# Kernel tuning notes

Hardware: AMD Instinct MI355X
Metric: run time of the kernel (lower is better)

## Reference

```python
import jax, jax.numpy as jnp
import numpy as np

W_ENTROPY, W_MI, W_COV, W_ORTHO, W_L1, W_L2 = 1.0, 0.2, 0.2, 0.1, 0.1, 0.1


def setup_inputs() -> dict:
    key = jax.random.key(0)
    k1, k2, k3, k4 = jax.random.split(key, 4)
    B, NCLS, C = 16384, 1000, 1280
    logits = jax.random.normal(k1, (B, NCLS), dtype=jnp.float32)
    output = jax.nn.log_softmax(logits, axis=1)  # nll_loss expects log-probs
    target = jax.random.randint(k2, (B,), 0, NCLS, dtype=jnp.int64)
    weights = jax.random.normal(k3, (NCLS, C), dtype=jnp.float32) * 0.02
    features = jax.random.normal(k4, (B, C), dtype=jnp.float32)
    return {"output": output, "target": target, "weights": weights, "features": features}


def _kl_loss(features):
    # torch: sum_{i,j} F.kl_div(L[:, i], L[:, j], log_target=True, reduction='mean')
    # kl_div(input, tgt, log_target=True) = mean_b exp(tgt)*(tgt - input)
    # => sum_{i,j,b} P[b,j]*(L[b,j]-L[b,i]) / B
    #  = (C * sum(P*L) - sum(L)) / B   (since sum_j P[b,j] == 1)
    B, C = features.shape
    L = jax.nn.log_softmax(features, axis=1)
    P = jnp.exp(L)
    return (C * jnp.sum(P * L) - jnp.sum(L)) / B


def _cov_loss(features):
    B = features.shape[0]
    cf = features - jnp.mean(features, axis=0, keepdims=True)
    cov = (cf.T @ cf) / B  # [C, C]
    eye = jnp.eye(cov.shape[0], dtype=cov.dtype)
    return jnp.sum((cov - eye) ** 2)  # ||.||_F^2


def _ortho_loss(weights):
    w = weights.reshape(weights.shape[0], -1)
    cov = w @ w.T  # row type
    eye = jnp.eye(cov.shape[0], dtype=cov.dtype)
    return jnp.sum((cov - eye) ** 2)


def reference(output, target, weights, features):
    loss_nll = -jnp.mean(jnp.take_along_axis(output, target[:, None], axis=1))
    loss_kl = _kl_loss(features)
    loss_cov = _cov_loss(features)
    loss_ortho = _ortho_loss(weights)
    loss_l1 = jnp.sum(jnp.abs(weights))
    loss_l2 = jnp.sqrt(jnp.sum(weights ** 2))
    loss = (W_ENTROPY * loss_nll + W_MI * loss_kl + W_COV * loss_cov
            + W_ORTHO * loss_ortho + W_L1 * loss_l1 + W_L2 * loss_l2)
    return loss
```

## Files before the change

### kernel.cpp

```cpp
#include <hip/hip_runtime.h>
#include <stdint.h>
#include <stddef.h>

#define B_N    16384
#define NCLS_N 1000
#define C_N    1280

#define ACC_OFF    0ULL
#define COLSUM_OFF 128ULL
#define FBT_OFF    8192ULL
#define WB_OFF     41951232ULL
#define G_OFF      44572672ULL
#define H_OFF      51126272ULL

enum { A_NLL = 0, A_KL = 1, A_L1 = 2, A_L2SQ = 3, A_SUMSQF = 4, A_FMU2 = 5, A_GFRO = 6, A_HFRO = 7 };

typedef short s16x8 __attribute__((ext_vector_type(8)));
typedef float f32x4 __attribute__((ext_vector_type(4)));

__device__ __forceinline__ unsigned short f2bf(float f) {
    union { float f; unsigned int u; } v; v.f = f;
    unsigned int u = v.u;
    u += 0x7fffu + ((u >> 16) & 1u);
    return (unsigned short)(u >> 16);
}

__device__ __forceinline__ float wave_red(float v) {
#pragma unroll
    for (int o = 32; o; o >>= 1) v += __shfl_down(v, o, 64);
    return v;
}


__device__ __forceinline__ void nll_body(const float* __restrict__ lp,
                                         const int* __restrict__ tgt,
                                         float* __restrict__ acc, int bidx) {
    int b = bidx * 256 + threadIdx.x;
    int t = tgt[b];
    float v = lp[(size_t)b * NCLS_N + t];
    v = wave_red(v);
    __shared__ float sm_nll[4];
    int wid = threadIdx.x >> 6, lane = threadIdx.x & 63;
    if (lane == 0) sm_nll[wid] = v;
    __syncthreads();
    if (threadIdx.x == 0) atomicAdd(&acc[A_NLL], sm_nll[0] + sm_nll[1] + sm_nll[2] + sm_nll[3]);
}

__device__ __forceinline__ void wpass_body(const float* __restrict__ W,
                                           short* __restrict__ Wb,
                                           float* __restrict__ acc, int idx) {
    int bx = idx & 3;
    int kc = idx >> 2;
    int m = bx * 256 + threadIdx.x;
    bool live = (m < NCLS_N);
    const float4* Wr = (const float4*)(W + (size_t)m * C_N);
    float l1 = 0.f, l2 = 0.f;
#pragma unroll
    for (int kj = 0; kj < 4; kj++) {
        s16x8 pk = { 0, 0, 0, 0, 0, 0, 0, 0 };
        if (live) {
            float4 a = Wr[kc * 8 + kj * 2];
            float4 b = Wr[kc * 8 + kj * 2 + 1];
            l1 += fabsf(a.x) + fabsf(a.y) + fabsf(a.z) + fabsf(a.w)
                + fabsf(b.x) + fabsf(b.y) + fabsf(b.z) + fabsf(b.w);
            l2 += a.x * a.x + a.y * a.y + a.z * a.z + a.w * a.w
                + b.x * b.x + b.y * b.y + b.z * b.z + b.w * b.w;
            pk[0] = (short)f2bf(a.x); pk[1] = (short)f2bf(a.y);
            pk[2] = (short)f2bf(a.z); pk[3] = (short)f2bf(a.w);
            pk[4] = (short)f2bf(b.x); pk[5] = (short)f2bf(b.y);
            pk[6] = (short)f2bf(b.z); pk[7] = (short)f2bf(b.w);
        }
        *(s16x8*)(Wb + ((size_t)(kc * 4 + kj) * 1024 + m) * 8) = pk;
    }
    l1 = wave_red(l1);
    l2 = wave_red(l2);
    __shared__ float sm_w[4][2];
    int wid = threadIdx.x >> 6, lane = threadIdx.x & 63;
    if (lane == 0) { sm_w[wid][0] = l1; sm_w[wid][1] = l2; }
    __syncthreads();
    if (threadIdx.x == 0) {
        atomicAdd(&acc[A_L1],   sm_w[0][0] + sm_w[1][0] + sm_w[2][0] + sm_w[3][0]);
        atomicAdd(&acc[A_L2SQ], sm_w[0][1] + sm_w[1][1] + sm_w[2][1] + sm_w[3][1]);
    }
}

__device__ __forceinline__ void fpass_body(const float* __restrict__ F,
                                           short* __restrict__ Fbt,
                                           float* __restrict__ colsum,
                                           float* __restrict__ acc, int idx) {
    int bx = idx % 5;
    int by = idx / 5;
    int c = bx * 256 + threadIdx.x;
    int kc0 = by * 4;
    float cs = 0.f, sq = 0.f;
    for (int ch = 0; ch < 4; ch++) {
        int kc = kc0 + ch;
        int kbase = kc * 32;
#pragma unroll
        for (int kj = 0; kj < 4; kj++) {
            float v[8];
#pragma unroll
            for (int e = 0; e < 8; e++) v[e] = F[(size_t)(kbase + kj * 8 + e) * C_N + c];
            s16x8 pk;
#pragma unroll
            for (int e = 0; e < 8; e++) {
                cs += v[e];
                sq += v[e] * v[e];
                pk[e] = (short)f2bf(v[e]);
            }
            *(s16x8*)(Fbt + ((size_t)(kc * 4 + kj) * C_N + c) * 8) = pk;
        }
    }
    atomicAdd(&colsum[c], cs);
    sq = wave_red(sq);
    __shared__ float sm_f[4];
    int wid = threadIdx.x >> 6, lane = threadIdx.x & 63;
    if (lane == 0) sm_f[wid] = sq;
    __syncthreads();
    if (threadIdx.x == 0) atomicAdd(&acc[A_SUMSQF], sm_f[0] + sm_f[1] + sm_f[2] + sm_f[3]);
}

__device__ __forceinline__ void klpass_body(const float* __restrict__ F,
                                            const float* __restrict__ colsum,
                                            float* __restrict__ acc, int idx) {
    int wid = threadIdx.x >> 6, lane = threadIdx.x & 63;
    int gwave = idx * 4 + wid;
    const float4* M = (const float4*)colsum;

    float kl_acc = 0.f, fmu_acc = 0.f;
    for (int b = gwave; b < B_N; b += 4096) {
        const float4* Fr = (const float4*)(F + (size_t)b * C_N);
        float s = 0.f, tt = 0.f, sf = 0.f, dp = 0.f;
#pragma unroll
        for (int i = 0; i < 5; i++) {
            float4 f = Fr[lane + 64 * i];
            float4 m = M[lane + 64 * i];
            float e0 = __expf(f.x), e1 = __expf(f.y), e2 = __expf(f.z), e3 = __expf(f.w);
            s  += e0 + e1 + e2 + e3;
            tt += e0 * f.x + e1 * f.y + e2 * f.z + e3 * f.w;
            sf += f.x + f.y + f.z + f.w;
            dp += f.x * m.x + f.y * m.y + f.z * m.z + f.w * m.w;
        }
        s = wave_red(s); tt = wave_red(tt); sf = wave_red(sf); dp = wave_red(dp);
        if (lane == 0) {
            kl_acc += (float)C_N * (tt / s) - sf;
            float dot = dp * (1.f / (float)B_N);
            fmu_acc += dot * dot;
        }
    }
    __shared__ float sm_kl[4][2];
    if (lane == 0) { sm_kl[wid][0] = kl_acc; sm_kl[wid][1] = fmu_acc; }
    __syncthreads();
    if (threadIdx.x == 0) {
        atomicAdd(&acc[A_KL],   sm_kl[0][0] + sm_kl[1][0] + sm_kl[2][0] + sm_kl[3][0]);
        atomicAdd(&acc[A_FMU2], sm_kl[0][1] + sm_kl[1][1] + sm_kl[2][1] + sm_kl[3][1]);
    }
}

__device__ __forceinline__ void gram_body(const short* __restrict__ X,
                                          float* __restrict__ S,
                                          int Mp, int T, int ntri, int chunkK, int bidx) {
    __shared__ __align__(16) short At[128 * 32];
    __shared__ __align__(16) short Bt[128 * 32];
    int tid = threadIdx.x;
    int tile = bidx % ntri;
    int kc_blk = bidx / ntri;
    int bi = 0, rem = tile;
    while (rem >= T - bi) { rem -= T - bi; bi++; }
    int bj = bi + rem;
    int i0 = bi * 128, j0 = bj * 128;
    int k0 = kc_blk * chunkK;
    bool same = (bi == bj);

    int wave = tid >> 6, lane = tid & 63;
    int wm = wave >> 1, wn = wave & 1;
    int quad = lane >> 4, l16 = lane & 15;

    f32x4 acc[4][4];
#pragma unroll
    for (int i = 0; i < 4; i++)
#pragma unroll
        for (int j = 0; j < 4; j++) acc[i][j] = { 0.f, 0.f, 0.f, 0.f };

    for (int kk = 0; kk < chunkK; kk += 32) {
        int kc = (k0 + kk) >> 5;
#pragma unroll
        for (int it = 0; it < 2; it++) {
            int g = it * 256 + tid;
            int row = g >> 2;
            int kj = (g & 3) ^ (row & 3);
            const short* gp = X + ((size_t)(kc * 4 + kj) * Mp + i0 + row) * 8;
            __builtin_amdgcn_global_load_lds((const __attribute__((address_space(1))) unsigned int*)gp,
                                             (__attribute__((address_space(3))) unsigned int*)(At + g * 8),
                                             16, 0, 0);
        }
        if (!same) {
#pragma unroll
            for (int it = 0; it < 2; it++) {
                int g = it * 256 + tid;
                int row = g >> 2;
                int kj = (g & 3) ^ (row & 3);
                const short* gp = X + ((size_t)(kc * 4 + kj) * Mp + j0 + row) * 8;
                __builtin_amdgcn_global_load_lds((const __attribute__((address_space(1))) unsigned int*)gp,
                                                 (__attribute__((address_space(3))) unsigned int*)(Bt + g * 8),
                                                 16, 0, 0);
            }
        }
        __syncthreads();
        const short* Bsrc = same ? At : Bt;
        s16x8 af[4], bfr[4];
#pragma unroll
        for (int f = 0; f < 4; f++) {
            int mrow = wm * 64 + f * 16 + l16;
            af[f] = *(const s16x8*)(At + mrow * 32 + (quad ^ (mrow & 3)) * 8);
            int nrow = wn * 64 + f * 16 + l16;
            bfr[f] = *(const s16x8*)(Bsrc + nrow * 32 + (quad ^ (nrow & 3)) * 8);
        }
#pragma unroll
        for (int i = 0; i < 4; i++)
#pragma unroll
            for (int j = 0; j < 4; j++)
                acc[i][j] = __builtin_amdgcn_mfma_f32_16x16x32_bf16(af[i], bfr[j], acc[i][j], 0, 0, 0);
        __syncthreads();
    }

#pragma unroll
    for (int i = 0; i < 4; i++)
#pragma unroll
        for (int j = 0; j < 4; j++)
#pragma unroll
            for (int r = 0; r < 4; r++) {
                int grow = i0 + wm * 64 + i * 16 + quad * 4 + r;
                int gcol = j0 + wn * 64 + j * 16 + l16;
                atomicAdd(&S[(size_t)grow * Mp + gcol], acc[i][j][r]);
            }
}

__device__ __forceinline__ void fro_tile(const float* __restrict__ S,
                                         int Mp, int T, int tile, float* __restrict__ slot) {
    int bi = 0, rem = tile;
    while (rem >= T - bi) { rem -= T - bi; bi++; }
    int bj = bi + rem;
    size_t base = (size_t)bi * 128 * Mp + (size_t)bj * 128;
    float sum = 0.f;
    for (int l = threadIdx.x * 4; l < 128 * 128; l += 1024) {
        int row = l >> 7, col = l & 127;
        float4 v = *(const float4*)(S + base + (size_t)row * Mp + col);
        sum += v.x * v.x + v.y * v.y + v.z * v.z + v.w * v.w;
    }
    sum = wave_red(sum);
    __shared__ float sm_fro[4];
    int wid = threadIdx.x >> 6, lane = threadIdx.x & 63;
    if (lane == 0) sm_fro[wid] = sum;
    __syncthreads();
    if (threadIdx.x == 0) {
        float w = (bi == bj) ? 1.f : 2.f;
        atomicAdd(slot, w * (sm_fro[0] + sm_fro[1] + sm_fro[2] + sm_fro[3]));
    }
}


__global__ __launch_bounds__(256) void prep_kernel(const float* __restrict__ lp,
                                                   const int* __restrict__ tgt,
                                                   const float* __restrict__ W,
                                                   const float* __restrict__ F,
                                                   short* __restrict__ Wb,
                                                   short* __restrict__ Fbt,
                                                   float* __restrict__ colsum,
                                                   float* __restrict__ acc,
                                                   float* __restrict__ G,
                                                   float* __restrict__ H) {
    int b = blockIdx.x;
    if (b < 64) {
        nll_body(lp, tgt, acc, b);
    } else if (b < 224) {
        wpass_body(W, Wb, acc, b - 64);
    } else if (b < 864) {
        fpass_body(F, Fbt, colsum, acc, b - 224);
    } else if (b < 964) {
        float4* p = (float4*)G + (size_t)(b - 864) * 4096;
        float4 z = { 0.f, 0.f, 0.f, 0.f };
        for (int i = threadIdx.x; i < 4096; i += 256) p[i] = z;
    } else {
        float4* p = (float4*)H + (size_t)(b - 964) * 4096;
        float4 z = { 0.f, 0.f, 0.f, 0.f };
        for (int i = threadIdx.x; i < 4096; i += 256) p[i] = z;
    }
}

__global__ __launch_bounds__(256) void main_kernel(const short* __restrict__ Fbt,
                                                   float* __restrict__ G,
                                                   const short* __restrict__ Wb,
                                                   float* __restrict__ H,
                                                   const float* __restrict__ F,
                                                   const float* __restrict__ colsum,
                                                   float* __restrict__ acc) {
    int b = blockIdx.x;
    if (b < 880) {
        gram_body(Fbt, G, C_N, 10, 55, 1024, b);
    } else if (b < 1904) {
        klpass_body(F, colsum, acc, b - 880);
    } else {
        gram_body(Wb, H, 1024, 8, 36, 320, b - 1904);
    }
}

__global__ __launch_bounds__(256) void fro_kernel(const float* __restrict__ G,
                                                  const float* __restrict__ H,
                                                  float* __restrict__ acc) {
    int b = blockIdx.x;
    if (b < 55) fro_tile(G, C_N, 10, b, acc + A_GFRO);
    else        fro_tile(H, 1024, 8, b - 55, acc + A_HFRO);
}

__global__ __launch_bounds__(256) void final_kernel(const float* __restrict__ acc,
                                                    const float* __restrict__ colsum,
                                                    float* __restrict__ out) {
    float s = 0.f;
    for (int c = threadIdx.x; c < C_N; c += 256) { float v = colsum[c]; s += v * v; }
    s = wave_red(s);
    __shared__ float sm[4];
    int wid = threadIdx.x >> 6, lane = threadIdx.x & 63;
    if (lane == 0) sm[wid] = s;
    __syncthreads();
    if (threadIdx.x == 0) {
        double musq_raw = (double)(sm[0] + sm[1] + sm[2] + sm[3]);
        double Bd = (double)B_N;
        double nll = -((double)acc[A_NLL] / Bd);
        double kl  = (double)acc[A_KL] / Bd;
        double trG = (double)acc[A_SUMSQF];
        double musq = musq_raw / (Bd * Bd);
        double cov = (double)acc[A_GFRO] / (Bd * Bd)
                   - (2.0 / Bd) * (double)acc[A_FMU2]
                   + musq * musq
                   - 2.0 * (trG / Bd - musq)
                   + (double)C_N;
        double ortho = (double)acc[A_HFRO] - 2.0 * (double)acc[A_L2SQ] + (double)NCLS_N;
        double loss = 1.0 * nll + 0.2 * kl + 0.2 * cov + 0.1 * ortho
                    + 0.1 * (double)acc[A_L1] + 0.1 * sqrt((double)acc[A_L2SQ]);
        out[0] = (float)loss;
    }
}

extern "C" void kernel_launch(void* const* d_in, const int* in_sizes, int n_in,
                              void* d_out, int out_size, void* d_ws, size_t ws_size,
                              hipStream_t stream) {
    (void)in_sizes; (void)n_in; (void)out_size; (void)ws_size;
    const float* output_lp = (const float*)d_in[0];
    const int*   target    = (const int*)d_in[1];
    const float* W         = (const float*)d_in[2];
    const float* F         = (const float*)d_in[3];

    char*  ws     = (char*)d_ws;
    float* acc    = (float*)(ws + ACC_OFF);
    float* colsum = (float*)(ws + COLSUM_OFF);
    short* Fbt    = (short*)(ws + FBT_OFF);
    short* Wb     = (short*)(ws + WB_OFF);
    float* G      = (float*)(ws + G_OFF);
    float* H      = (float*)(ws + H_OFF);

    hipMemsetAsync(ws, 0, 8192, stream);

    prep_kernel<<<1028, 256, 0, stream>>>(output_lp, target, W, F, Wb, Fbt, colsum, acc, G, H);
    main_kernel<<<2048, 256, 0, stream>>>(Fbt, G, Wb, H, F, colsum, acc);
    fro_kernel<<<91, 256, 0, stream>>>(G, H, acc);
    final_kernel<<<1, 256, 0, stream>>>(acc, colsum, (float*)d_out);
}
```

Measured before the change: 297.3 us.

## Double-buffer gram LDS loads, split F pass finer, fuse fro and final kernels

The gram GEMM now uses ping-pong LDS buffers, so the global-to-LDS loads for the next K step are issued while MFMAs run on the current one. Global pointers are precomputed and advanced by a fixed stride each step. The feature conversion pass is split into four times as many blocks (one 32-row chunk each), and the prep kernel's branch order is rearranged. The final reduction is folded into the fro kernel through an atomic ticket that the last block uses to compute the loss, which removes one launch. The costs are doubled LDS per block, which may lower occupancy, and more colsum atomics.

```diff
diff --git a/kernel.cpp b/kernel.cpp
--- a/kernel.cpp
+++ b/kernel.cpp
@@ -7,6 +7,7 @@
 #define C_N    1280
 
 #define ACC_OFF    0ULL
+#define TICKET_OFF 64ULL
 #define COLSUM_OFF 128ULL
 #define FBT_OFF    8192ULL
 #define WB_OFF     41951232ULL
@@ -89,27 +90,23 @@
                                            float* __restrict__ colsum,
                                            float* __restrict__ acc, int idx) {
     int bx = idx % 5;
-    int by = idx / 5;
+    int kc = idx / 5;
     int c = bx * 256 + threadIdx.x;
-    int kc0 = by * 4;
+    int kbase = kc * 32;
     float cs = 0.f, sq = 0.f;
-    for (int ch = 0; ch < 4; ch++) {
-        int kc = kc0 + ch;
-        int kbase = kc * 32;
-#pragma unroll
-        for (int kj = 0; kj < 4; kj++) {
-            float v[8];
-#pragma unroll
-            for (int e = 0; e < 8; e++) v[e] = F[(size_t)(kbase + kj * 8 + e) * C_N + c];
-            s16x8 pk;
-#pragma unroll
-            for (int e = 0; e < 8; e++) {
-                cs += v[e];
-                sq += v[e] * v[e];
-                pk[e] = (short)f2bf(v[e]);
-            }
-            *(s16x8*)(Fbt + ((size_t)(kc * 4 + kj) * C_N + c) * 8) = pk;
-        }
+#pragma unroll
+    for (int kj = 0; kj < 4; kj++) {
+        float v[8];
+#pragma unroll
+        for (int e = 0; e < 8; e++) v[e] = F[(size_t)(kbase + kj * 8 + e) * C_N + c];
+        s16x8 pk;
+#pragma unroll
+        for (int e = 0; e < 8; e++) {
+            cs += v[e];
+            sq += v[e] * v[e];
+            pk[e] = (short)f2bf(v[e]);
+        }
+        *(s16x8*)(Fbt + ((size_t)(kc * 4 + kj) * C_N + c) * 8) = pk;
     }
     atomicAdd(&colsum[c], cs);
     sq = wave_red(sq);
@@ -160,8 +157,10 @@
 __device__ __forceinline__ void gram_body(const short* __restrict__ X,
                                           float* __restrict__ S,
                                           int Mp, int T, int ntri, int chunkK, int bidx) {
-    __shared__ __align__(16) short At[128 * 32];
-    __shared__ __align__(16) short Bt[128 * 32];
+    __shared__ __align__(16) short A0[128 * 32];
+    __shared__ __align__(16) short A1[128 * 32];
+    __shared__ __align__(16) short B0[128 * 32];
+    __shared__ __align__(16) short B1[128 * 32];
     int tid = threadIdx.x;
     int tile = bidx % ntri;
     int kc_blk = bidx / ntri;
@@ -169,58 +168,71 @@
     while (rem >= T - bi) { rem -= T - bi; bi++; }
     int bj = bi + rem;
     int i0 = bi * 128, j0 = bj * 128;
-    int k0 = kc_blk * chunkK;
     bool same = (bi == bj);
 
     int wave = tid >> 6, lane = tid & 63;
     int wm = wave >> 1, wn = wave & 1;
     int quad = lane >> 4, l16 = lane & 15;
 
+    const size_t kstep = (size_t)Mp * 32;
+    const short *pa0, *pa1, *pb0, *pb1;
+    int lo0 = tid * 8, lo1 = (256 + tid) * 8;
+    {
+        int g0 = tid, g1 = 256 + tid;
+        int r0 = g0 >> 2, r1 = g1 >> 2;
+        int kj0 = (g0 & 3) ^ (r0 & 3), kj1 = (g1 & 3) ^ (r1 & 3);
+        size_t base = (size_t)(kc_blk * chunkK >> 5) * kstep;
+        pa0 = X + base + ((size_t)kj0 * Mp + i0 + r0) * 8;
+        pa1 = X + base + ((size_t)kj1 * Mp + i0 + r1) * 8;
+        pb0 = X + base + ((size_t)kj0 * Mp + j0 + r0) * 8;
+        pb1 = X + base + ((size_t)kj1 * Mp + j0 + r1) * 8;
+    }
+
     f32x4 acc[4][4];
 #pragma unroll
     for (int i = 0; i < 4; i++)
 #pragma unroll
         for (int j = 0; j < 4; j++) acc[i][j] = { 0.f, 0.f, 0.f, 0.f };
 
-    for (int kk = 0; kk < chunkK; kk += 32) {
-        int kc = (k0 + kk) >> 5;
-#pragma unroll
-        for (int it = 0; it < 2; it++) {
-            int g = it * 256 + tid;
-            int row = g >> 2;
-            int kj = (g & 3) ^ (row & 3);
-            const short* gp = X + ((size_t)(kc * 4 + kj) * Mp + i0 + row) * 8;
-            __builtin_amdgcn_global_load_lds((const __attribute__((address_space(1))) unsigned int*)gp,
-                                             (__attribute__((address_space(3))) unsigned int*)(At + g * 8),
-                                             16, 0, 0);
-        }
+    auto stage = [&](short* Ad, short* Bd) {
+        __builtin_amdgcn_global_load_lds((const __attribute__((address_space(1))) unsigned int*)pa0,
+                                         (__attribute__((address_space(3))) unsigned int*)(Ad + lo0), 16, 0, 0);
+        __builtin_amdgcn_global_load_lds((const __attribute__((address_space(1))) unsigned int*)pa1,
+                                         (__attribute__((address_space(3))) unsigned int*)(Ad + lo1), 16, 0, 0);
         if (!same) {
-#pragma unroll
-            for (int it = 0; it < 2; it++) {
-                int g = it * 256 + tid;
-                int row = g >> 2;
-                int kj = (g & 3) ^ (row & 3);
-                const short* gp = X + ((size_t)(kc * 4 + kj) * Mp + j0 + row) * 8;
-                __builtin_amdgcn_global_load_lds((const __attribute__((address_space(1))) unsigned int*)gp,
-                                                 (__attribute__((address_space(3))) unsigned int*)(Bt + g * 8),
-                                                 16, 0, 0);
-            }
-        }
-        __syncthreads();
-        const short* Bsrc = same ? At : Bt;
+            __builtin_amdgcn_global_load_lds((const __attribute__((address_space(1))) unsigned int*)pb0,
+                                             (__attribute__((address_space(3))) unsigned int*)(Bd + lo0), 16, 0, 0);
+            __builtin_amdgcn_global_load_lds((const __attribute__((address_space(1))) unsigned int*)pb1,
+                                             (__attribute__((address_space(3))) unsigned int*)(Bd + lo1), 16, 0, 0);
+        }
+        pa0 += kstep; pa1 += kstep; pb0 += kstep; pb1 += kstep;
+    };
+
+    auto compute = [&](const short* Ab, const short* Bb) {
         s16x8 af[4], bfr[4];
 #pragma unroll
         for (int f = 0; f < 4; f++) {
             int mrow = wm * 64 + f * 16 + l16;
-            af[f] = *(const s16x8*)(At + mrow * 32 + (quad ^ (mrow & 3)) * 8);
+            af[f] = *(const s16x8*)(Ab + mrow * 32 + (quad ^ (mrow & 3)) * 8);
             int nrow = wn * 64 + f * 16 + l16;
-            bfr[f] = *(const s16x8*)(Bsrc + nrow * 32 + (quad ^ (nrow & 3)) * 8);
+            bfr[f] = *(const s16x8*)(Bb + nrow * 32 + (quad ^ (nrow & 3)) * 8);
         }
 #pragma unroll
         for (int i = 0; i < 4; i++)
 #pragma unroll
             for (int j = 0; j < 4; j++)
                 acc[i][j] = __builtin_amdgcn_mfma_f32_16x16x32_bf16(af[i], bfr[j], acc[i][j], 0, 0, 0);
+    };
+
+    int nt = chunkK >> 5;
+    stage(A0, B0);
+    __syncthreads();
+    for (int t = 0; t < nt; t += 2) {
+        stage(A1, B1);
+        compute(A0, same ? A0 : B0);
+        __syncthreads();
+        if (t + 2 < nt) stage(A0, B0);
+        compute(A1, same ? A1 : B1);
         __syncthreads();
     }
 
@@ -271,18 +283,18 @@
                                                    float* __restrict__ G,
                                                    float* __restrict__ H) {
     int b = blockIdx.x;
-    if (b < 64) {
-        nll_body(lp, tgt, acc, b);
-    } else if (b < 224) {
-        wpass_body(W, Wb, acc, b - 64);
-    } else if (b < 864) {
-        fpass_body(F, Fbt, colsum, acc, b - 224);
-    } else if (b < 964) {
-        float4* p = (float4*)G + (size_t)(b - 864) * 4096;
+    if (b < 2560) {
+        fpass_body(F, Fbt, colsum, acc, b);
+    } else if (b < 2720) {
+        wpass_body(W, Wb, acc, b - 2560);
+    } else if (b < 2784) {
+        nll_body(lp, tgt, acc, b - 2720);
+    } else if (b < 2884) {
+        float4* p = (float4*)G + (size_t)(b - 2784) * 4096;
         float4 z = { 0.f, 0.f, 0.f, 0.f };
         for (int i = threadIdx.x; i < 4096; i += 256) p[i] = z;
     } else {
-        float4* p = (float4*)H + (size_t)(b - 964) * 4096;
+        float4* p = (float4*)H + (size_t)(b - 2884) * 4096;
         float4 z = { 0.f, 0.f, 0.f, 0.f };
         for (int i = threadIdx.x; i < 4096; i += 256) p[i] = z;
     }
@@ -305,17 +317,26 @@
     }
 }
 
-__global__ __launch_bounds__(256) void fro_kernel(const float* __restrict__ G,
-                                                  const float* __restrict__ H,
-                                                  float* __restrict__ acc) {
+__global__ __launch_bounds__(256) void fro_final_kernel(const float* __restrict__ G,
+                                                        const float* __restrict__ H,
+                                                        float* __restrict__ acc,
+                                                        const float* __restrict__ colsum,
+                                                        unsigned* __restrict__ ticket,
+                                                        float* __restrict__ out) {
     int b = blockIdx.x;
     if (b < 55) fro_tile(G, C_N, 10, b, acc + A_GFRO);
     else        fro_tile(H, 1024, 8, b - 55, acc + A_HFRO);
-}
-
-__global__ __launch_bounds__(256) void final_kernel(const float* __restrict__ acc,
-                                                    const float* __restrict__ colsum,
-                                                    float* __restrict__ out) {
+
+    __shared__ int amlast;
+    if (threadIdx.x == 0) {
+        __threadfence();
+        unsigned prev = atomicAdd(ticket, 1u);
+        amlast = (prev == 90u);
+    }
+    __syncthreads();
+    if (!amlast) return;
+    __threadfence();
+
     float s = 0.f;
     for (int c = threadIdx.x; c < C_N; c += 256) { float v = colsum[c]; s += v * v; }
     s = wave_red(s);
@@ -326,16 +347,18 @@
     if (threadIdx.x == 0) {
         double musq_raw = (double)(sm[0] + sm[1] + sm[2] + sm[3]);
         double Bd = (double)B_N;
+        double gfro = (double)atomicAdd(&acc[A_GFRO], 0.0f);
+        double hfro = (double)atomicAdd(&acc[A_HFRO], 0.0f);
         double nll = -((double)acc[A_NLL] / Bd);
         double kl  = (double)acc[A_KL] / Bd;
         double trG = (double)acc[A_SUMSQF];
         double musq = musq_raw / (Bd * Bd);
-        double cov = (double)acc[A_GFRO] / (Bd * Bd)
+        double cov = gfro / (Bd * Bd)
                    - (2.0 / Bd) * (double)acc[A_FMU2]
                    + musq * musq
                    - 2.0 * (trG / Bd - musq)
                    + (double)C_N;
-        double ortho = (double)acc[A_HFRO] - 2.0 * (double)acc[A_L2SQ] + (double)NCLS_N;
+        double ortho = hfro - 2.0 * (double)acc[A_L2SQ] + (double)NCLS_N;
         double loss = 1.0 * nll + 0.2 * kl + 0.2 * cov + 0.1 * ortho
                     + 0.1 * (double)acc[A_L1] + 0.1 * sqrt((double)acc[A_L2SQ]);
         out[0] = (float)loss;
@@ -351,18 +374,18 @@
     const float* W         = (const float*)d_in[2];
     const float* F         = (const float*)d_in[3];
 
-    char*  ws     = (char*)d_ws;
-    float* acc    = (float*)(ws + ACC_OFF);
-    float* colsum = (float*)(ws + COLSUM_OFF);
-    short* Fbt    = (short*)(ws + FBT_OFF);
-    short* Wb     = (short*)(ws + WB_OFF);
-    float* G      = (float*)(ws + G_OFF);
-    float* H      = (float*)(ws + H_OFF);
+    char*     ws     = (char*)d_ws;
+    float*    acc    = (float*)(ws + ACC_OFF);
+    unsigned* ticket = (unsigned*)(ws + TICKET_OFF);
+    float*    colsum = (float*)(ws + COLSUM_OFF);
+    short*    Fbt    = (short*)(ws + FBT_OFF);
+    short*    Wb     = (short*)(ws + WB_OFF);
+    float*    G      = (float*)(ws + G_OFF);
+    float*    H      = (float*)(ws + H_OFF);
 
     hipMemsetAsync(ws, 0, 8192, stream);
 
-    prep_kernel<<<1028, 256, 0, stream>>>(output_lp, target, W, F, Wb, Fbt, colsum, acc, G, H);
+    prep_kernel<<<2948, 256, 0, stream>>>(output_lp, target, W, F, Wb, Fbt, colsum, acc, G, H);
     main_kernel<<<2048, 256, 0, stream>>>(Fbt, G, Wb, H, F, colsum, acc);
-    fro_kernel<<<91, 256, 0, stream>>>(G, H, acc);
-    final_kernel<<<1, 256, 0, stream>>>(acc, colsum, (float*)d_out);
-}
+    fro_final_kernel<<<91, 256, 0, stream>>>(G, H, acc, colsum, ticket, (float*)d_out);
+}
```

New measurement: 309.5 us. 4.1% more time.
